# Kernel tuning notes

Hardware: AMD Instinct MI355X
Metric: run time of the kernel (lower is better)

The kernel has to match this reference:

```python
import jax, jax.numpy as jnp
import numpy as np

B, N, L, C = 4, 16, 192, 64
H = 128
ROW, COL = 16, 12  # L == ROW*COL, ROW >= COL
NUM = 2  # class_num


def setup_inputs() -> dict:
    key = jax.random.key(0)
    ks = jax.random.split(key, 12)
    s = 1.0 / np.sqrt(H).astype(np.float32)
    u = lambda k, shape: jax.random.uniform(k, shape, jnp.float32, -s, s)
    return {
        "x": jax.random.normal(ks[0], (B, N, L, C), jnp.float32),
        "pad_mask": jnp.ones((B, N), jnp.bool_),
        "fc3_w": u(ks[1], (H, C)), "fc3_b": u(ks[2], (H,)),
        "fc4_w": u(ks[3], (H, H)), "fc4_b": u(ks[4], (H,)),
        "W_enc": u(ks[5], (NUM, 6 * H, 3 * H)), "B_enc": u(ks[6], (NUM, 6 * H)),
        "fc1_w": u(ks[7], (NUM, 1, H)), "fc1_b": u(ks[8], (NUM, 1)),
        "fc2_w": u(ks[9], (NUM, 1, H)), "fc2_b": u(ks[10], (NUM, 1)),
    }


def _witran_encoder(a, W, Bb):
    # a: [COL*BN, slice_len, H] diagonally-shifted input; W: [6H, 3H]; Bb: [6H]
    RBN, slice_len, _ = a.shape
    BN = RBN // COL
    R = COL  # Water2sea_slice_num (after permute(2,0,1,3), slices run over col)
    slice_ids = jnp.arange(RBN) // BN
    xs = jnp.transpose(a, (1, 0, 2))  # [slice_len, RBN, H]

    def step(carry, inp):
        h_row, h_col = carry
        x_s, s = inp
        g = jnp.concatenate([h_row, h_col, x_s], axis=-1) @ W.T  # [RBN, 6H]
        # torch adds bias only to first batch*(s+1) rows, and only while s < slice_num
        mask = (slice_ids <= s) & (s < R)
        g = g + jnp.where(mask[:, None], Bb, jnp.zeros((), g.dtype))
        sig = jax.nn.sigmoid(g[:, : 4 * H])
        th = jnp.tanh(g[:, 4 * H:])
        u_r, o_r, u_c, o_c = jnp.split(sig, 4, axis=-1)
        i_r, i_c = jnp.split(th, 2, axis=-1)
        h_row = jnp.tanh((1 - u_r) * h_row + u_r * i_r) * o_r
        h_col = jnp.tanh((1 - u_c) * h_col + u_c * i_c) * o_c
        # saved pieces (only valid for late s; we keep the last, which is always valid)
        loc = jnp.clip(s - ROW + 1, 0, R - 1)
        row_save = jax.lax.dynamic_slice_in_dim(h_row, loc * BN, BN, axis=0)
        col_save = h_col[(R - 1) * BN:, :]  # save BEFORE roll, as in torch
        h_col = jnp.roll(h_col, BN, axis=0)
        return (h_row, h_col), (row_save, col_save)

    h0 = jnp.zeros((RBN, H), a.dtype)
    (_, _), (row_saves, col_saves) = jax.lax.scan(
        step, (h0, h0), (xs, jnp.arange(slice_len)))
    # last entries == hidden_row_all[:, -1, -1, :], hidden_col_all[:, -1, -1, :]
    return row_saves[-1], col_saves[-1]  # each [BN, H]


def reference(x, pad_mask, fc3_w, fc3_b, fc4_w, fc4_b, W_enc, B_enc,
              fc1_w, fc1_b, fc2_w, fc2_b):
    Bn, Nn = x.shape[0], x.shape[1]
    h = jax.nn.relu(x @ fc3_w.T + fc3_b) @ fc4_w.T + fc4_b  # [B,N,L,H]
    xr = h.reshape(-1, ROW, COL, H)          # [BN, row, col, H]
    inp = jnp.transpose(xr, (2, 0, 1, 3))    # [col, BN, row, H]
    slice_len = COL + ROW - 1
    # diagonal 'water2sea' shift: transfer[r, :, r:r+ROW] = inp[r]
    padded = jnp.pad(inp, ((0, 0), (0, 0), (0, COL - 1), (0, 0)))
    transfer = jax.vmap(lambda t, r: jnp.roll(t, r, axis=1))(padded, jnp.arange(COL))
    a = transfer.reshape(COL * Bn * Nn, slice_len, H)

    def per_class(W, Bb, f1w, f1b, f2w, f2b):
        row_last, col_last = _witran_encoder(a, W, Bb)
        # torch: row := hidden_col_all tail, col := hidden_row_all tail
        out = 0.5 * (col_last @ f1w.T + f1b) + 0.5 * (row_last @ f2w.T + f2b)
        return out[:, 0]  # [BN]

    y = jax.vmap(per_class)(W_enc, B_enc, fc1_w, fc1_b, fc2_w, fc2_b)  # [NUM, BN]
    return jnp.transpose(y).reshape(Bn, Nn, NUM)
```

## Files before the change

kernel.cpp:

```cpp
#include <hip/hip_runtime.h>

typedef _Float16 hf;
typedef _Float16 half2v __attribute__((ext_vector_type(2)));
typedef _Float16 half8 __attribute__((ext_vector_type(8)));
typedef float f32x4 __attribute__((ext_vector_type(4)));
typedef int int4v __attribute__((ext_vector_type(4)));

constexpr int Steps = 27;

constexpr int OFF_WX = 393216;
constexpr int OFF_F3 = 589824;
constexpr int OFF_F4 = 598016;
constexpr int OFF_XW = 614400;

__device__ __forceinline__ int aidx(int r, int k) {
  int blk = k >> 3;
  return r * 256 + (((blk ^ (r & 7)) & 31) << 3) + (k & 7);
}
__device__ __forceinline__ int hidx(int r, int k) {
  int blk = k >> 3;
  return r * 128 + (((blk ^ (r & 15)) & 15) << 3) + (k & 7);
}
__device__ __forceinline__ int xidx(int r, int k) {
  int blk = k >> 3;
  return r * 64 + (((blk ^ (r & 7)) & 7) << 3) + (k & 7);
}
__device__ __forceinline__ float rcpf_(float x) { return __builtin_amdgcn_rcpf(x); }
__device__ __forceinline__ float sigmoidf_(float x) { return rcpf_(1.0f + __expf(-x)); }
__device__ __forceinline__ float tanh_(float x) { return 1.0f - 2.0f * rcpf_(__expf(2.0f * x) + 1.0f); }

__device__ __forceinline__ int bar_dep() {
  int z;
  __builtin_amdgcn_sched_barrier(0);
  asm volatile("s_waitcnt lgkmcnt(0)\n\ts_barrier\n\ts_mov_b32 %0, 0" : "=s"(z));
  __builtin_amdgcn_sched_barrier(0);
  return z;
}

__global__ __launch_bounds__(512) void prep(const float* __restrict__ fc3_w,
                                            const float* __restrict__ fc4_w,
                                            const float* __restrict__ W_enc,
                                            hf* __restrict__ wsh) {
  int idx = (blockIdx.x * 512 + threadIdx.x) * 8;
  if (idx >= OFF_XW) return;
  const float* src;
  if (idx < OFF_WX) {
    int lane = (idx >> 3) & 63, rest = idx >> 9;
    int ks = rest & 7; rest >>= 3;
    int j = rest % 3; rest /= 3;
    int wv = rest & 15, cls = rest >> 4;
    int gate = (wv < 8) ? (j < 2 ? j : 4) : (j < 2 ? j + 2 : 5);
    int n = gate * 128 + (wv & 7) * 16 + (lane & 15);
    int k = ks * 32 + ((lane >> 4) << 3);
    src = W_enc + (size_t)(cls * 768 + n) * 384 + k;
  } else if (idx < OFF_F3) {
    int f = idx - OFF_WX;
    int lane = (f >> 3) & 63, rest = f >> 9;
    int ks = rest & 3; rest >>= 2;
    int wv = rest & 7; rest >>= 3;
    int gate = rest % 6, cls = rest / 6;
    int n = gate * 128 + wv * 16 + (lane & 15);
    int k = 256 + ks * 32 + ((lane >> 4) << 3);
    src = W_enc + (size_t)(cls * 768 + n) * 384 + k;
  } else if (idx < OFF_F4) {
    int f = idx - OFF_F3;
    int lane = (f >> 3) & 63, rest = f >> 9;
    int ks = rest & 1, wv = rest >> 1;
    int n = wv * 16 + (lane & 15), k = ks * 32 + ((lane >> 4) << 3);
    src = fc3_w + n * 64 + k;
  } else {
    int f = idx - OFF_F4;
    int lane = (f >> 3) & 63, rest = f >> 9;
    int ks = rest & 3, wv = rest >> 2;
    int n = wv * 16 + (lane & 15), k = ks * 32 + ((lane >> 4) << 3);
    src = fc4_w + n * 128 + k;
  }
  f32x4 a = *(const f32x4*)src, b = *(const f32x4*)(src + 4);
  half8 h;
  h[0] = (hf)a.x; h[1] = (hf)a.y; h[2] = (hf)a.z; h[3] = (hf)a.w;
  h[4] = (hf)b.x; h[5] = (hf)b.y; h[6] = (hf)b.z; h[7] = (hf)b.w;
  *(half8*)&wsh[idx] = h;
}

__global__ __launch_bounds__(512) void prelude(
    const float* __restrict__ x, const float* __restrict__ fc3_b, const float* __restrict__ fc4_b,
    const float* __restrict__ B_enc, const hf* __restrict__ wsh, hf* __restrict__ xWb) {
  const int t = threadIdx.x, lane = t & 63, wv = t >> 6;
  const int c16 = lane & 15, quad = lane >> 4;
  const int row0 = blockIdx.x * 64, bn = row0 / 192, l0 = row0 % 192;
  const int d = wv * 16 + c16;

  __shared__ __attribute__((aligned(16))) hf xA[64 * 64];
  __shared__ __attribute__((aligned(16))) hf hbuf[64 * 128];
  __shared__ __attribute__((aligned(16))) hf xout[64 * 768];
  __shared__ float actf[64];

  {
    int r = t >> 3, cb = (t & 7) * 8;
    const float* xp = x + (size_t)(row0 + r) * 64 + cb;
    f32x4 a = *(const f32x4*)xp, b = *(const f32x4*)(xp + 4);
    half8 h;
    h[0] = (hf)a.x; h[1] = (hf)a.y; h[2] = (hf)a.z; h[3] = (hf)a.w;
    h[4] = (hf)b.x; h[5] = (hf)b.y; h[6] = (hf)b.z; h[7] = (hf)b.w;
    *(half8*)&xA[xidx(r, cb)] = h;
  }
  if (t < 64) {
    int l = l0 + t;
    actf[t] = ((l / 12) + (l % 12)) < 12 ? 1.f : 0.f;
  }
  __syncthreads();

  {
    float b3v = fc3_b[d];
    half8 w0 = *(const half8*)(wsh + OFF_F3 + (wv * 2 + 0) * 512 + lane * 8);
    half8 w1 = *(const half8*)(wsh + OFF_F3 + (wv * 2 + 1) * 512 + lane * 8);
    f32x4 acc[4] = {{0, 0, 0, 0}, {0, 0, 0, 0}, {0, 0, 0, 0}, {0, 0, 0, 0}};
#pragma unroll
    for (int mt = 0; mt < 4; ++mt) {
      half8 a0 = *(const half8*)&xA[xidx(mt * 16 + c16, quad * 8)];
      half8 a1 = *(const half8*)&xA[xidx(mt * 16 + c16, 32 + quad * 8)];
      acc[mt] = __builtin_amdgcn_mfma_f32_16x16x32_f16(a0, w0, acc[mt], 0, 0, 0);
      acc[mt] = __builtin_amdgcn_mfma_f32_16x16x32_f16(a1, w1, acc[mt], 0, 0, 0);
    }
#pragma unroll
    for (int mt = 0; mt < 4; ++mt)
#pragma unroll
      for (int r = 0; r < 4; ++r)
        hbuf[hidx(mt * 16 + quad * 4 + r, d)] = (hf)fmaxf(acc[mt][r] + b3v, 0.f);
  }
  __syncthreads();

  {
    float b4v = fc4_b[d];
    half8 w4[4];
#pragma unroll
    for (int ks = 0; ks < 4; ++ks)
      w4[ks] = *(const half8*)(wsh + OFF_F4 + (wv * 4 + ks) * 512 + lane * 8);
    f32x4 acc[4] = {{0, 0, 0, 0}, {0, 0, 0, 0}, {0, 0, 0, 0}, {0, 0, 0, 0}};
#pragma unroll
    for (int mt = 0; mt < 4; ++mt)
#pragma unroll
      for (int ks = 0; ks < 4; ++ks) {
        half8 a = *(const half8*)&hbuf[hidx(mt * 16 + c16, ks * 32 + quad * 8)];
        acc[mt] = __builtin_amdgcn_mfma_f32_16x16x32_f16(a, w4[ks], acc[mt], 0, 0, 0);
      }
    __syncthreads();
#pragma unroll
    for (int mt = 0; mt < 4; ++mt)
#pragma unroll
      for (int r = 0; r < 4; ++r)
        hbuf[hidx(mt * 16 + quad * 4 + r, d)] = (hf)(acc[mt][r] + b4v);
  }
  __syncthreads();

  half8 af[4][4];
#pragma unroll
  for (int mt = 0; mt < 4; ++mt)
#pragma unroll
    for (int ks = 0; ks < 4; ++ks)
      af[mt][ks] = *(const half8*)&hbuf[hidx(mt * 16 + c16, ks * 32 + quad * 8)];

  for (int cls = 0; cls < 2; ++cls) {
    for (int g = 0; g < 6; ++g) {
      int pos = (g < 2) ? g : (g < 4 ? g + 1 : (g == 4 ? 2 : 5));
      half8 wf[4];
#pragma unroll
      for (int ks = 0; ks < 4; ++ks)
        wf[ks] = *(const half8*)(wsh + OFF_WX + (((cls * 6 + g) * 8 + wv) * 4 + ks) * 512 + lane * 8);
      float bv = B_enc[cls * 768 + g * 128 + d];
#pragma unroll
      for (int mt = 0; mt < 4; ++mt) {
        f32x4 acc = {0.f, 0.f, 0.f, 0.f};
#pragma unroll
        for (int ks = 0; ks < 4; ++ks)
          acc = __builtin_amdgcn_mfma_f32_16x16x32_f16(af[mt][ks], wf[ks], acc, 0, 0, 0);
#pragma unroll
        for (int r = 0; r < 4; ++r) {
          int row = mt * 16 + quad * 4 + r;
          xout[row * 768 + d * 6 + pos] = (hf)(acc[r] + actf[row] * bv);
        }
      }
    }
    __syncthreads();
    {
      const int* src = (const int*)xout;
      int* dst = (int*)(xWb + (((size_t)cls * 64 + bn) * 192 + l0) * 768);
#pragma unroll
      for (int i = 0; i < 12; ++i) {
        int base = (t + i * 512) * 4;
        *(int4v*)&dst[base] = *(const int4v*)&src[base];
      }
    }
    __syncthreads();
  }
}

__device__ __forceinline__ float lo16f(unsigned v) {
  return (float)__builtin_bit_cast(half2v, v)[0];
}
__device__ __forceinline__ float hi16f(unsigned v) {
  return (float)__builtin_bit_cast(half2v, v)[1];
}

__global__ __launch_bounds__(512, 2) __attribute__((amdgpu_waves_per_eu(2, 2))) void witran(
    const hf* __restrict__ wsh, const float* __restrict__ fc1_w, const float* __restrict__ fc1_b,
    const float* __restrict__ fc2_w, const float* __restrict__ fc2_b,
    const hf* __restrict__ xWb, float* __restrict__ out) {
  const int cls = blockIdx.x & 1, bn = blockIdx.x >> 1;
  const int t = threadIdx.x, lane = t & 63, wv = t >> 6;
  const int c16 = lane & 15, quad = lane >> 4;
  const int d = wv * 16 + c16;
  const bool act = (quad < 3);
  const int c0 = quad * 4;

  __shared__ __attribute__((aligned(16))) hf wlds[8 * 4096];
  __shared__ __attribute__((aligned(16))) hf A[2][4096];
  __shared__ float red[128];

  for (int i = t; i < 4096; i += 512) ((int*)A)[i] = 0;

  half8 wf[5][8];
  {
    const hf* wbR = wsh + ((size_t)((cls * 16 + wv) * 3) * 8) * 512 + lane * 8;
    const hf* wbC = wsh + ((size_t)((cls * 16 + 8 + wv) * 3) * 8) * 512 + lane * 8;
#pragma unroll
    for (int j = 0; j < 3; ++j)
#pragma unroll
      for (int ks = 0; ks < 8; ++ks)
        wf[j][ks] = *(const half8*)(wbR + (j * 8 + ks) * 512);
#pragma unroll
    for (int j = 0; j < 2; ++j)
#pragma unroll
      for (int ks = 0; ks < 8; ++ks)
        wf[3 + j][ks] = *(const half8*)(wbC + (j * 8 + ks) * 512);
#pragma unroll
    for (int ks = 0; ks < 8; ++ks)
      *(half8*)&wlds[wv * 4096 + ks * 512 + lane * 8] = *(const half8*)(wbC + (16 + ks) * 512);
  }

  const hf* xg = xWb + ((size_t)cls * 64 + bn) * 192 * 768;
  int xrun = d * 12 - c0 * 16896;
  unsigned pxc[4][3];
  float hr[4] = {0.f, 0.f, 0.f, 0.f};

  auto xload = [&](int s) {
#pragma unroll
    for (int r = 0; r < 4; ++r) {
      int c = c0 + r;
      bool ok = act && ((unsigned)(s - c) < 16u);
      int off = ok ? (xrun - r * 16896) : 0;
      const hf* p = (const hf*)((const char*)xg + off);
      pxc[r][0] = *(const unsigned*)p;
      pxc[r][1] = *(const unsigned*)(p + 2);
      pxc[r][2] = *(const unsigned*)(p + 4);
    }
    xrun += 18432;
  };

  auto step = [&](const hf* Ac0, hf* An0, int s, int zk) -> int {
    const hf* Ac = Ac0 + zk;
    hf* An = An0 + zk;
    float hcold[4];
#pragma unroll
    for (int r = 0; r < 4; ++r) hcold[r] = (float)Ac[aidx(c0 + r, 128 + d)];
    f32x4 acc[6];
#pragma unroll
    for (int g = 0; g < 6; ++g) acc[g] = (f32x4){0.f, 0.f, 0.f, 0.f};
#pragma unroll
    for (int ks = 0; ks < 8; ++ks) {
      half8 av = *(const half8*)&Ac[aidx(c16, ks * 32 + quad * 8)];
#pragma unroll
      for (int g = 0; g < 5; ++g)
        acc[g] = __builtin_amdgcn_mfma_f32_16x16x32_f16(av, wf[g][ks], acc[g], 0, 0, 0);
      half8 w5 = *(const half8*)&wlds[zk + wv * 4096 + ks * 512 + lane * 8];
      acc[5] = __builtin_amdgcn_mfma_f32_16x16x32_f16(av, w5, acc[5], 0, 0, 0);
    }
    if (act) {
#pragma unroll
      for (int r = 0; r < 4; ++r) {
        int c = c0 + r;
        bool okx = ((unsigned)(s - c) < 16u);
        unsigned v0 = okx ? pxc[r][0] : 0u;
        unsigned v1 = okx ? pxc[r][1] : 0u;
        unsigned v2 = okx ? pxc[r][2] : 0u;
        float xur = lo16f(v0), xor_ = hi16f(v0);
        float xir = lo16f(v1), xuc = hi16f(v1);
        float xoc = lo16f(v2), xic = hi16f(v2);
        float uu = sigmoidf_(acc[0][r] + xur);
        float oo = sigmoidf_(acc[1][r] + xor_);
        float ii = tanh_(acc[2][r] + xir);
        float h1 = tanh_(hr[r] + uu * (ii - hr[r])) * oo;
        hr[r] = h1;
        An[aidx(c, d)] = (hf)h1;
        float u2 = sigmoidf_(acc[3][r] + xuc);
        float o2 = sigmoidf_(acc[4][r] + xoc);
        float i2 = tanh_(acc[5][r] + xic);
        float h2 = tanh_(hcold[r] + u2 * (i2 - hcold[r])) * o2;
        int cw = (c == 11) ? 0 : c + 1;
        An[aidx(cw, 128 + d)] = (hf)h2;
      }
    }
    xload(s + 1);
    return bar_dep();
  };

  xload(0);
  int zk = bar_dep();

#pragma unroll 1
  for (int s = 0; s < Steps - 1; s += 2) {
    zk = step(A[0], A[1], s, zk);
    zk = step(A[1], A[0], s + 1, zk);
  }
  zk = step(A[0], A[1], Steps - 1, zk);

  const hf* Af = A[1] + zk;
  if (t < 128) {
    float hrv = (float)Af[aidx(11, t)];
    float hcv = (float)Af[aidx(0, 128 + t)];
    red[t] = 0.5f * (hcv * fc1_w[cls * 128 + t] + hrv * fc2_w[cls * 128 + t]);
  }
  __syncthreads();
  if (t == 0) {
    float sum = 0.f;
    for (int i = 0; i < 128; ++i) sum += red[i];
    out[bn * 2 + cls] = sum + 0.5f * (fc1_b[cls] + fc2_b[cls]);
  }
}

extern "C" void kernel_launch(void* const* d_in, const int* in_sizes, int n_in,
                              void* d_out, int out_size, void* d_ws, size_t ws_size,
                              hipStream_t stream) {
  const float* x = (const float*)d_in[0];
  const float* fc3_w = (const float*)d_in[2];
  const float* fc3_b = (const float*)d_in[3];
  const float* fc4_w = (const float*)d_in[4];
  const float* fc4_b = (const float*)d_in[5];
  const float* W_enc = (const float*)d_in[6];
  const float* B_enc = (const float*)d_in[7];
  const float* fc1_w = (const float*)d_in[8];
  const float* fc1_b = (const float*)d_in[9];
  const float* fc2_w = (const float*)d_in[10];
  const float* fc2_b = (const float*)d_in[11];
  float* out = (float*)d_out;

  hf* wsh = (hf*)d_ws;
  hf* xWb = wsh + OFF_XW;

  prep<<<dim3(150), dim3(512), 0, stream>>>(fc3_w, fc4_w, W_enc, wsh);
  prelude<<<dim3(192), dim3(512), 0, stream>>>(x, fc3_b, fc4_b, B_enc, wsh, xWb);
  witran<<<dim3(128), dim3(512), 0, stream>>>(wsh, fc1_w, fc1_b, fc2_w, fc2_b, xWb, out);
}
```

Baseline: 163.7 us.

## Fuse prelude MLP and input projection into the recurrent witran kernel

Removes the separate prelude kernel. Each witran block now computes the fc3/fc4 MLP for its own bn's 192 positions into shared memory. Inside each recurrent step it then computes the input-gate projection with extra MFMAs, reading weights from global memory, instead of reading a precomputed xWb buffer. This saves a kernel launch and the global write/read of the large projected tensor. In exchange, each of the two class blocks recomputes the MLP, and every sequential step does more MFMA work and global weight loads, lengthening the latency-bound recurrence.

```diff
diff --git a/kernel.cpp b/kernel.cpp
--- a/kernel.cpp
+++ b/kernel.cpp
@@ -2,9 +2,9 @@
 
 typedef _Float16 hf;
 typedef _Float16 half2v __attribute__((ext_vector_type(2)));
+typedef _Float16 half4 __attribute__((ext_vector_type(4)));
 typedef _Float16 half8 __attribute__((ext_vector_type(8)));
 typedef float f32x4 __attribute__((ext_vector_type(4)));
-typedef int int4v __attribute__((ext_vector_type(4)));
 
 constexpr int Steps = 27;
 
@@ -12,6 +12,15 @@
 constexpr int OFF_F3 = 589824;
 constexpr int OFF_F4 = 598016;
 constexpr int OFF_XW = 614400;
+
+constexpr int H_OFF = 0;
+constexpr int R_OFF = 24704;
+constexpr int XA_OFF = R_OFF;
+constexpr int H1_OFF = R_OFF + 12288;
+constexpr int A0_OFF = R_OFF;
+constexpr int A1_OFF = R_OFF + 4096;
+constexpr int WL_OFF = R_OFF + 8192;
+constexpr int SM_HALFS = R_OFF + 40960;
 
 __device__ __forceinline__ int aidx(int r, int k) {
   int blk = k >> 3;
@@ -82,130 +91,13 @@
   *(half8*)&wsh[idx] = h;
 }
 
-__global__ __launch_bounds__(512) void prelude(
-    const float* __restrict__ x, const float* __restrict__ fc3_b, const float* __restrict__ fc4_b,
-    const float* __restrict__ B_enc, const hf* __restrict__ wsh, hf* __restrict__ xWb) {
-  const int t = threadIdx.x, lane = t & 63, wv = t >> 6;
-  const int c16 = lane & 15, quad = lane >> 4;
-  const int row0 = blockIdx.x * 64, bn = row0 / 192, l0 = row0 % 192;
-  const int d = wv * 16 + c16;
-
-  __shared__ __attribute__((aligned(16))) hf xA[64 * 64];
-  __shared__ __attribute__((aligned(16))) hf hbuf[64 * 128];
-  __shared__ __attribute__((aligned(16))) hf xout[64 * 768];
-  __shared__ float actf[64];
-
-  {
-    int r = t >> 3, cb = (t & 7) * 8;
-    const float* xp = x + (size_t)(row0 + r) * 64 + cb;
-    f32x4 a = *(const f32x4*)xp, b = *(const f32x4*)(xp + 4);
-    half8 h;
-    h[0] = (hf)a.x; h[1] = (hf)a.y; h[2] = (hf)a.z; h[3] = (hf)a.w;
-    h[4] = (hf)b.x; h[5] = (hf)b.y; h[6] = (hf)b.z; h[7] = (hf)b.w;
-    *(half8*)&xA[xidx(r, cb)] = h;
-  }
-  if (t < 64) {
-    int l = l0 + t;
-    actf[t] = ((l / 12) + (l % 12)) < 12 ? 1.f : 0.f;
-  }
-  __syncthreads();
-
-  {
-    float b3v = fc3_b[d];
-    half8 w0 = *(const half8*)(wsh + OFF_F3 + (wv * 2 + 0) * 512 + lane * 8);
-    half8 w1 = *(const half8*)(wsh + OFF_F3 + (wv * 2 + 1) * 512 + lane * 8);
-    f32x4 acc[4] = {{0, 0, 0, 0}, {0, 0, 0, 0}, {0, 0, 0, 0}, {0, 0, 0, 0}};
-#pragma unroll
-    for (int mt = 0; mt < 4; ++mt) {
-      half8 a0 = *(const half8*)&xA[xidx(mt * 16 + c16, quad * 8)];
-      half8 a1 = *(const half8*)&xA[xidx(mt * 16 + c16, 32 + quad * 8)];
-      acc[mt] = __builtin_amdgcn_mfma_f32_16x16x32_f16(a0, w0, acc[mt], 0, 0, 0);
-      acc[mt] = __builtin_amdgcn_mfma_f32_16x16x32_f16(a1, w1, acc[mt], 0, 0, 0);
-    }
-#pragma unroll
-    for (int mt = 0; mt < 4; ++mt)
-#pragma unroll
-      for (int r = 0; r < 4; ++r)
-        hbuf[hidx(mt * 16 + quad * 4 + r, d)] = (hf)fmaxf(acc[mt][r] + b3v, 0.f);
-  }
-  __syncthreads();
-
-  {
-    float b4v = fc4_b[d];
-    half8 w4[4];
-#pragma unroll
-    for (int ks = 0; ks < 4; ++ks)
-      w4[ks] = *(const half8*)(wsh + OFF_F4 + (wv * 4 + ks) * 512 + lane * 8);
-    f32x4 acc[4] = {{0, 0, 0, 0}, {0, 0, 0, 0}, {0, 0, 0, 0}, {0, 0, 0, 0}};
-#pragma unroll
-    for (int mt = 0; mt < 4; ++mt)
-#pragma unroll
-      for (int ks = 0; ks < 4; ++ks) {
-        half8 a = *(const half8*)&hbuf[hidx(mt * 16 + c16, ks * 32 + quad * 8)];
-        acc[mt] = __builtin_amdgcn_mfma_f32_16x16x32_f16(a, w4[ks], acc[mt], 0, 0, 0);
-      }
-    __syncthreads();
-#pragma unroll
-    for (int mt = 0; mt < 4; ++mt)
-#pragma unroll
-      for (int r = 0; r < 4; ++r)
-        hbuf[hidx(mt * 16 + quad * 4 + r, d)] = (hf)(acc[mt][r] + b4v);
-  }
-  __syncthreads();
-
-  half8 af[4][4];
-#pragma unroll
-  for (int mt = 0; mt < 4; ++mt)
-#pragma unroll
-    for (int ks = 0; ks < 4; ++ks)
-      af[mt][ks] = *(const half8*)&hbuf[hidx(mt * 16 + c16, ks * 32 + quad * 8)];
-
-  for (int cls = 0; cls < 2; ++cls) {
-    for (int g = 0; g < 6; ++g) {
-      int pos = (g < 2) ? g : (g < 4 ? g + 1 : (g == 4 ? 2 : 5));
-      half8 wf[4];
-#pragma unroll
-      for (int ks = 0; ks < 4; ++ks)
-        wf[ks] = *(const half8*)(wsh + OFF_WX + (((cls * 6 + g) * 8 + wv) * 4 + ks) * 512 + lane * 8);
-      float bv = B_enc[cls * 768 + g * 128 + d];
-#pragma unroll
-      for (int mt = 0; mt < 4; ++mt) {
-        f32x4 acc = {0.f, 0.f, 0.f, 0.f};
-#pragma unroll
-        for (int ks = 0; ks < 4; ++ks)
-          acc = __builtin_amdgcn_mfma_f32_16x16x32_f16(af[mt][ks], wf[ks], acc, 0, 0, 0);
-#pragma unroll
-        for (int r = 0; r < 4; ++r) {
-          int row = mt * 16 + quad * 4 + r;
-          xout[row * 768 + d * 6 + pos] = (hf)(acc[r] + actf[row] * bv);
-        }
-      }
-    }
-    __syncthreads();
-    {
-      const int* src = (const int*)xout;
-      int* dst = (int*)(xWb + (((size_t)cls * 64 + bn) * 192 + l0) * 768);
-#pragma unroll
-      for (int i = 0; i < 12; ++i) {
-        int base = (t + i * 512) * 4;
-        *(int4v*)&dst[base] = *(const int4v*)&src[base];
-      }
-    }
-    __syncthreads();
-  }
-}
-
-__device__ __forceinline__ float lo16f(unsigned v) {
-  return (float)__builtin_bit_cast(half2v, v)[0];
-}
-__device__ __forceinline__ float hi16f(unsigned v) {
-  return (float)__builtin_bit_cast(half2v, v)[1];
-}
-
 __global__ __launch_bounds__(512, 2) __attribute__((amdgpu_waves_per_eu(2, 2))) void witran(
-    const hf* __restrict__ wsh, const float* __restrict__ fc1_w, const float* __restrict__ fc1_b,
+    const hf* __restrict__ wsh, const float* __restrict__ x,
+    const float* __restrict__ fc3_b, const float* __restrict__ fc4_b,
+    const float* __restrict__ B_enc,
+    const float* __restrict__ fc1_w, const float* __restrict__ fc1_b,
     const float* __restrict__ fc2_w, const float* __restrict__ fc2_b,
-    const hf* __restrict__ xWb, float* __restrict__ out) {
+    float* __restrict__ out) {
   const int cls = blockIdx.x & 1, bn = blockIdx.x >> 1;
   const int t = threadIdx.x, lane = t & 63, wv = t >> 6;
   const int c16 = lane & 15, quad = lane >> 4;
@@ -213,11 +105,7 @@
   const bool act = (quad < 3);
   const int c0 = quad * 4;
 
-  __shared__ __attribute__((aligned(16))) hf wlds[8 * 4096];
-  __shared__ __attribute__((aligned(16))) hf A[2][4096];
-  __shared__ float red[128];
-
-  for (int i = t; i < 4096; i += 512) ((int*)A)[i] = 0;
+  __shared__ __attribute__((aligned(16))) hf smem[SM_HALFS];
 
   half8 wf[5][8];
   {
@@ -233,36 +121,91 @@
 #pragma unroll
       for (int ks = 0; ks < 8; ++ks)
         wf[3 + j][ks] = *(const half8*)(wbC + (j * 8 + ks) * 512);
+  }
+  float bv[6];
+  {
+    const int G[6] = {0, 1, 4, 2, 3, 5};
+#pragma unroll
+    for (int j = 0; j < 6; ++j) bv[j] = B_enc[cls * 768 + G[j] * 128 + d];
+  }
+
+#pragma unroll
+  for (int i = 0; i < 6; ++i) {
+    int f = t * 4 + i * 2048;
+    int r = f >> 6, cb = f & 63;
+    f32x4 a = *(const f32x4*)(x + (size_t)(bn * 192 + r) * 64 + cb);
+    half4 h4;
+    h4[0] = (hf)a.x; h4[1] = (hf)a.y; h4[2] = (hf)a.z; h4[3] = (hf)a.w;
+    *(half4*)&smem[XA_OFF + xidx(r, cb)] = h4;
+  }
+  if (t < 16) {
+    half8 z = {};
+    *(half8*)&smem[H_OFF + 192 * 128 + t * 8] = z;
+  }
+  __syncthreads();
+
+  {
+    float b3v = fc3_b[d];
+    half8 w0 = *(const half8*)(wsh + OFF_F3 + (wv * 2 + 0) * 512 + lane * 8);
+    half8 w1 = *(const half8*)(wsh + OFF_F3 + (wv * 2 + 1) * 512 + lane * 8);
+#pragma unroll
+    for (int mt = 0; mt < 12; ++mt) {
+      f32x4 a = {0.f, 0.f, 0.f, 0.f};
+      a = __builtin_amdgcn_mfma_f32_16x16x32_f16(
+          *(const half8*)&smem[XA_OFF + xidx(mt * 16 + c16, quad * 8)], w0, a, 0, 0, 0);
+      a = __builtin_amdgcn_mfma_f32_16x16x32_f16(
+          *(const half8*)&smem[XA_OFF + xidx(mt * 16 + c16, 32 + quad * 8)], w1, a, 0, 0, 0);
+#pragma unroll
+      for (int r = 0; r < 4; ++r)
+        smem[H1_OFF + hidx(mt * 16 + quad * 4 + r, d)] = (hf)fmaxf(a[r] + b3v, 0.f);
+    }
+  }
+  __syncthreads();
+
+  {
+    float b4v = fc4_b[d];
+    half8 w4[4];
+#pragma unroll
+    for (int ks = 0; ks < 4; ++ks)
+      w4[ks] = *(const half8*)(wsh + OFF_F4 + (wv * 4 + ks) * 512 + lane * 8);
+#pragma unroll
+    for (int mt = 0; mt < 12; ++mt) {
+      f32x4 a = {0.f, 0.f, 0.f, 0.f};
+#pragma unroll
+      for (int ks = 0; ks < 4; ++ks)
+        a = __builtin_amdgcn_mfma_f32_16x16x32_f16(
+            *(const half8*)&smem[H1_OFF + hidx(mt * 16 + c16, ks * 32 + quad * 8)], w4[ks], a,
+            0, 0, 0);
+#pragma unroll
+      for (int r = 0; r < 4; ++r)
+        smem[H_OFF + hidx(mt * 16 + quad * 4 + r, d)] = (hf)(a[r] + b4v);
+    }
+  }
+  __syncthreads();
+
+  for (int i = t; i < 4096; i += 512) ((int*)&smem[A0_OFF])[i] = 0;
+  {
+    const hf* wbC = wsh + ((size_t)((cls * 16 + 8 + wv) * 3) * 8) * 512 + lane * 8;
 #pragma unroll
     for (int ks = 0; ks < 8; ++ks)
-      *(half8*)&wlds[wv * 4096 + ks * 512 + lane * 8] = *(const half8*)(wbC + (16 + ks) * 512);
-  }
-
-  const hf* xg = xWb + ((size_t)cls * 64 + bn) * 192 * 768;
-  int xrun = d * 12 - c0 * 16896;
-  unsigned pxc[4][3];
+      *(half8*)&smem[WL_OFF + wv * 4096 + ks * 512 + lane * 8] =
+          *(const half8*)(wbC + (16 + ks) * 512);
+  }
+
+  const hf* wxs = wsh + OFF_WX + (size_t)(cls * 48 + wv) * 2048 + lane * 8;
+
   float hr[4] = {0.f, 0.f, 0.f, 0.f};
 
-  auto xload = [&](int s) {
-#pragma unroll
-    for (int r = 0; r < 4; ++r) {
-      int c = c0 + r;
-      bool ok = act && ((unsigned)(s - c) < 16u);
-      int off = ok ? (xrun - r * 16896) : 0;
-      const hf* p = (const hf*)((const char*)xg + off);
-      pxc[r][0] = *(const unsigned*)p;
-      pxc[r][1] = *(const unsigned*)(p + 2);
-      pxc[r][2] = *(const unsigned*)(p + 4);
-    }
-    xrun += 18432;
-  };
-
-  auto step = [&](const hf* Ac0, hf* An0, int s, int zk) -> int {
-    const hf* Ac = Ac0 + zk;
-    hf* An = An0 + zk;
-    float hcold[4];
-#pragma unroll
-    for (int r = 0; r < 4; ++r) hcold[r] = (float)Ac[aidx(c0 + r, 128 + d)];
+  auto step = [&](int acof, int anof, int s, int zk_) -> int {
+    const hf* Ac = smem + acof + zk_;
+    hf* An = smem + anof + zk_;
+    const hf* wxp = wxs + zk_;
+    half8 wxA[8];
+#pragma unroll
+    for (int ks = 0; ks < 4; ++ks) {
+      wxA[ks] = *(const half8*)(wxp + 0 * 16384 + ks * 512);
+      wxA[4 + ks] = *(const half8*)(wxp + 1 * 16384 + ks * 512);
+    }
     f32x4 acc[6];
 #pragma unroll
     for (int g = 0; g < 6; ++g) acc[g] = (f32x4){0.f, 0.f, 0.f, 0.f};
@@ -272,49 +215,82 @@
 #pragma unroll
       for (int g = 0; g < 5; ++g)
         acc[g] = __builtin_amdgcn_mfma_f32_16x16x32_f16(av, wf[g][ks], acc[g], 0, 0, 0);
-      half8 w5 = *(const half8*)&wlds[zk + wv * 4096 + ks * 512 + lane * 8];
+      half8 w5 = *(const half8*)&smem[WL_OFF + zk_ + wv * 4096 + ks * 512 + lane * 8];
       acc[5] = __builtin_amdgcn_mfma_f32_16x16x32_f16(av, w5, acc[5], 0, 0, 0);
     }
+    unsigned rrv = (unsigned)(s - c16);
+    int cell = (c16 < 12 && rrv < 16u) ? (int)rrv * 12 + c16 : 192;
+    half8 avx[4];
+#pragma unroll
+    for (int ks = 0; ks < 4; ++ks)
+      avx[ks] = *(const half8*)&smem[H_OFF + hidx(cell, ks * 32 + quad * 8)];
+#pragma unroll
+    for (int ks = 0; ks < 4; ++ks)
+      acc[0] = __builtin_amdgcn_mfma_f32_16x16x32_f16(avx[ks], wxA[ks], acc[0], 0, 0, 0);
+#pragma unroll
+    for (int ks = 0; ks < 4; ++ks)
+      acc[1] = __builtin_amdgcn_mfma_f32_16x16x32_f16(avx[ks], wxA[4 + ks], acc[1], 0, 0, 0);
+    half8 wxB[8];
+#pragma unroll
+    for (int ks = 0; ks < 4; ++ks) {
+      wxB[ks] = *(const half8*)(wxp + 4 * 16384 + ks * 512);
+      wxB[4 + ks] = *(const half8*)(wxp + 2 * 16384 + ks * 512);
+    }
+#pragma unroll
+    for (int ks = 0; ks < 4; ++ks)
+      acc[2] = __builtin_amdgcn_mfma_f32_16x16x32_f16(avx[ks], wxB[ks], acc[2], 0, 0, 0);
+#pragma unroll
+    for (int ks = 0; ks < 4; ++ks)
+      acc[3] = __builtin_amdgcn_mfma_f32_16x16x32_f16(avx[ks], wxB[4 + ks], acc[3], 0, 0, 0);
+    half8 wxC[8];
+#pragma unroll
+    for (int ks = 0; ks < 4; ++ks) {
+      wxC[ks] = *(const half8*)(wxp + 3 * 16384 + ks * 512);
+      wxC[4 + ks] = *(const half8*)(wxp + 5 * 16384 + ks * 512);
+    }
+#pragma unroll
+    for (int ks = 0; ks < 4; ++ks)
+      acc[4] = __builtin_amdgcn_mfma_f32_16x16x32_f16(avx[ks], wxC[ks], acc[4], 0, 0, 0);
+#pragma unroll
+    for (int ks = 0; ks < 4; ++ks)
+      acc[5] = __builtin_amdgcn_mfma_f32_16x16x32_f16(avx[ks], wxC[4 + ks], acc[5], 0, 0, 0);
     if (act) {
+      float hcold[4];
+#pragma unroll
+      for (int r = 0; r < 4; ++r) hcold[r] = (float)Ac[aidx(c0 + r, 128 + d)];
 #pragma unroll
       for (int r = 0; r < 4; ++r) {
         int c = c0 + r;
         bool okx = ((unsigned)(s - c) < 16u);
-        unsigned v0 = okx ? pxc[r][0] : 0u;
-        unsigned v1 = okx ? pxc[r][1] : 0u;
-        unsigned v2 = okx ? pxc[r][2] : 0u;
-        float xur = lo16f(v0), xor_ = hi16f(v0);
-        float xir = lo16f(v1), xuc = hi16f(v1);
-        float xoc = lo16f(v2), xic = hi16f(v2);
-        float uu = sigmoidf_(acc[0][r] + xur);
-        float oo = sigmoidf_(acc[1][r] + xor_);
-        float ii = tanh_(acc[2][r] + xir);
+        float bm = (okx && s < 12) ? 1.f : 0.f;
+        float uu = sigmoidf_(acc[0][r] + bm * bv[0]);
+        float oo = sigmoidf_(acc[1][r] + bm * bv[1]);
+        float ii = tanh_(acc[2][r] + bm * bv[2]);
         float h1 = tanh_(hr[r] + uu * (ii - hr[r])) * oo;
         hr[r] = h1;
         An[aidx(c, d)] = (hf)h1;
-        float u2 = sigmoidf_(acc[3][r] + xuc);
-        float o2 = sigmoidf_(acc[4][r] + xoc);
-        float i2 = tanh_(acc[5][r] + xic);
+        float u2 = sigmoidf_(acc[3][r] + bm * bv[3]);
+        float o2 = sigmoidf_(acc[4][r] + bm * bv[4]);
+        float i2 = tanh_(acc[5][r] + bm * bv[5]);
         float h2 = tanh_(hcold[r] + u2 * (i2 - hcold[r])) * o2;
         int cw = (c == 11) ? 0 : c + 1;
         An[aidx(cw, 128 + d)] = (hf)h2;
       }
     }
-    xload(s + 1);
     return bar_dep();
   };
 
-  xload(0);
   int zk = bar_dep();
 
 #pragma unroll 1
   for (int s = 0; s < Steps - 1; s += 2) {
-    zk = step(A[0], A[1], s, zk);
-    zk = step(A[1], A[0], s + 1, zk);
-  }
-  zk = step(A[0], A[1], Steps - 1, zk);
-
-  const hf* Af = A[1] + zk;
+    zk = step(A0_OFF, A1_OFF, s, zk);
+    zk = step(A1_OFF, A0_OFF, s + 1, zk);
+  }
+  zk = step(A0_OFF, A1_OFF, Steps - 1, zk);
+
+  const hf* Af = smem + A1_OFF + zk;
+  float* red = (float*)&smem[H_OFF];
   if (t < 128) {
     float hrv = (float)Af[aidx(11, t)];
     float hcv = (float)Af[aidx(0, 128 + t)];
@@ -345,9 +321,8 @@
   float* out = (float*)d_out;
 
   hf* wsh = (hf*)d_ws;
-  hf* xWb = wsh + OFF_XW;
 
   prep<<<dim3(150), dim3(512), 0, stream>>>(fc3_w, fc4_w, W_enc, wsh);
-  prelude<<<dim3(192), dim3(512), 0, stream>>>(x, fc3_b, fc4_b, B_enc, wsh, xWb);
-  witran<<<dim3(128), dim3(512), 0, stream>>>(wsh, fc1_w, fc1_b, fc2_w, fc2_b, xWb, out);
-}
+  witran<<<dim3(128), dim3(512), 0, stream>>>(wsh, x, fc3_b, fc4_b, B_enc,
+                                              fc1_w, fc1_b, fc2_w, fc2_b, out);
+}
```

Measured after the change: 202.1 us. +23.4%, slower.
